# Performance work log

Measured on AMD Instinct MI355X. Metric: run time of the kernel, lower is better.

## Reference

```python
import jax, jax.numpy as jnp
import numpy as np

B, T = 2, 1024
V, D, H, L = 32000, 1024, 16, 8
DH = D // H  # 64
ROPE_BASE = 1000.0
EPS = 1e-6


def _rms_norm(x):
    # F.rms_norm(x, (C,), eps=1e-6)
    ms = jnp.mean(jnp.square(x), axis=-1, keepdims=True)
    return x * jax.lax.rsqrt(ms + EPS)


def _rope_tables(t_len):
    quarter = DH // 4
    inv_freq = jnp.concatenate([
        ROPE_BASE ** (-jnp.arange(quarter, dtype=jnp.float32) / quarter),
        jnp.zeros(quarter, dtype=jnp.float32),
    ])  # [DH/2]
    theta = jnp.arange(t_len, dtype=jnp.float32)[:, None] * inv_freq[None, :]  # [T, DH/2]
    return jnp.cos(theta), jnp.sin(theta)


def _apply_rope(x, cos, sin):
    # x: [B, H, T, DH]; cos/sin: [T, DH/2] broadcast to [1,1,T,DH/2]
    half = DH // 2
    x1, x2 = x[..., :half], x[..., half:]
    c = cos[None, None]
    s = sin[None, None]
    return jnp.concatenate([c * x1 - s * x2, s * x1 + c * x2], axis=-1).astype(x.dtype)


def setup_inputs() -> dict:
    key = jax.random.key(0)
    ks = jax.random.split(key, 7)
    s = 0.02
    return {
        "x_indices": jax.random.randint(ks[0], (B, T), 0, V, dtype=jnp.int32),
        "embedding": jax.random.normal(ks[1], (V, D), dtype=jnp.float32) * s,
        "Wqkv": jax.random.normal(ks[2], (L, 3 * D, D), dtype=jnp.float32) * s,
        "Wout": jax.random.normal(ks[3], (L, D, D), dtype=jnp.float32) * s,
        "W1": jax.random.normal(ks[4], (L, 4 * D, D), dtype=jnp.float32) * s,
        "W2": jax.random.normal(ks[5], (L, D, 4 * D), dtype=jnp.float32) * s,
        "lm_head": jax.random.normal(ks[6], (V, D), dtype=jnp.float32) * s,
    }


def reference(x_indices, embedding, Wqkv, Wout, W1, W2, lm_head):
    x = embedding[x_indices]  # [B, T, D]
    cos, sin = _rope_tables(T)
    causal = jnp.tril(jnp.ones((T, T), dtype=bool))  # [T, T]
    neg = jnp.finfo(x.dtype).min
    scale = 1.0 / np.sqrt(DH)

    for l in range(L):
        n = _rms_norm(x)
        qkv = jnp.einsum('btd,ed->bte', n, Wqkv[l])  # [B, T, 3D]
        qkv = qkv.reshape(B, T, 3, H, DH)
        q = jnp.transpose(qkv[:, :, 0], (0, 2, 1, 3))  # [B, H, T, DH]
        k = jnp.transpose(qkv[:, :, 1], (0, 2, 1, 3))
        v = jnp.transpose(qkv[:, :, 2], (0, 2, 1, 3))
        q = _apply_rope(q, cos, sin)
        k = _apply_rope(k, cos, sin)
        scores = jnp.einsum('bhqd,bhkd->bhqk', q, k) * scale
        scores = jnp.where(causal[None, None], scores, neg)
        attn = jax.nn.softmax(scores, axis=-1)
        ctx = jnp.einsum('bhqk,bhkd->bhqd', attn, v)
        ctx = jnp.transpose(ctx, (0, 2, 1, 3)).reshape(B, T, D)
        x = x + jnp.einsum('btd,ed->bte', ctx, Wout[l])
        n = _rms_norm(x)
        h = jnp.square(jax.nn.relu(jnp.einsum('btd,fd->btf', n, W1[l])))  # [B, T, 4D]
        x = x + jnp.einsum('btf,df->btd', h, W2[l])

    logits = jnp.einsum('btd,vd->btv', _rms_norm(x), lm_head)
    return logits.astype(jnp.float32)
```

## Files before the change

kernel.cpp:

```cpp
#include <hip/hip_runtime.h>
#include <hip/hip_bf16.h>
#include <cmath>
#include <cstdint>

#define B_  2
#define T_  1024
#define V_  32000
#define D_  1024
#define H_  16
#define L_  8
#define DH_ 64

typedef __attribute__((ext_vector_type(8))) short bf16x8;
typedef __attribute__((ext_vector_type(4))) float f32x4;

__device__ __forceinline__ ushort f2bf(float f) {
    union { float f; uint32_t u; } v; v.f = f;
    uint32_t r = v.u + 0x7FFFu + ((v.u >> 16) & 1u);
    return (ushort)(r >> 16);
}
__device__ __forceinline__ float bf2f(ushort u) {
    union { uint32_t u; float f; } v; v.u = ((uint32_t)u) << 16;
    return v.f;
}

__device__ __forceinline__ void async_copy16(const void* g, void* l) {
    __builtin_amdgcn_global_load_lds(
        (const __attribute__((address_space(1))) void*)g,
        (__attribute__((address_space(3))) void*)l, 16, 0, 0);
}

__global__ __launch_bounds__(256) void k_cast(const float4* __restrict__ in,
                                              ushort4* __restrict__ out, int n4) {
    for (int i = blockIdx.x * 256 + threadIdx.x; i < n4; i += gridDim.x * 256) {
        float4 v = in[i];
        out[i] = make_ushort4(f2bf(v.x), f2bf(v.y), f2bf(v.z), f2bf(v.w));
    }
}

__global__ void k_rope_tables(float* __restrict__ cosT, float* __restrict__ sinT) {
    int t = blockIdx.x;
    int i = threadIdx.x;
    float invf = (i < 16) ? powf(1000.0f, -(float)i / 16.0f) : 0.0f;
    float th = (float)t * invf;
    cosT[t * 32 + i] = cosf(th);
    sinT[t * 32 + i] = sinf(th);
}

__global__ __launch_bounds__(256) void k_gather(const int* __restrict__ idx,
                                                const float* __restrict__ emb,
                                                float* __restrict__ x) {
    int row = blockIdx.x;
    int id = idx[row];
    const float4* src = (const float4*)(emb + (size_t)id * D_);
    float4* dst = (float4*)(x + (size_t)row * D_);
    dst[threadIdx.x] = src[threadIdx.x];
}

__global__ __launch_bounds__(256) void k_rmsnorm(const float* __restrict__ x,
                                                 ushort* __restrict__ out) {
    int row = blockIdx.x;
    const float4* xr = (const float4*)(x + (size_t)row * D_);
    float4 v = xr[threadIdx.x];
    float ss = v.x * v.x + v.y * v.y + v.z * v.z + v.w * v.w;
    #pragma unroll
    for (int off = 1; off < 64; off <<= 1) ss += __shfl_xor(ss, off);
    __shared__ float wsum[4];
    int lane = threadIdx.x & 63, wv = threadIdx.x >> 6;
    if (lane == 0) wsum[wv] = ss;
    __syncthreads();
    float tot = wsum[0] + wsum[1] + wsum[2] + wsum[3];
    float inv = rsqrtf(tot * (1.0f / D_) + 1e-6f);
    ushort4 r = make_ushort4(f2bf(v.x * inv), f2bf(v.y * inv), f2bf(v.z * inv), f2bf(v.w * inv));
    *(ushort4*)(out + (size_t)row * D_ + threadIdx.x * 4) = r;
}

template<int BN, int EPI, bool OUTBF, bool CONVB>
__global__ __launch_bounds__(256, 2) void k_mfma_gemm(const ushort* __restrict__ A,
                                                      const void* __restrict__ Wp,
                                                      void* __restrict__ Cp,
                                                      const float* __restrict__ Res,
                                                      const float* __restrict__ cosT,
                                                      const float* __restrict__ sinT,
                                                      int M, int N, int K) {
    constexpr int BM = 128;
    constexpr int MI = 4;
    constexpr int NI = BN / 32;
    constexpr bool DBUF = (BN <= 128);
    constexpr int NB = DBUF ? 2 : 1;
    __shared__ ushort As[NB][BM][64];
    __shared__ ushort Bs[NB][BN][64];
    const int tid = threadIdx.x;
    const int wid = tid >> 6, lane = tid & 63;
    const int wr = wid >> 1, wc = wid & 1;
    const int r16 = lane & 15, kc = lane >> 4;
    const int rx = (r16 & 7) << 4;
    const int srow8 = tid >> 3;
    const int sdcp = tid & 7;

    const int nwg = gridDim.x * gridDim.y;
    int orig = blockIdx.y * gridDim.x + blockIdx.x;
    int swz = (nwg & 7) ? orig : ((orig & 7) * (nwg >> 3) + (orig >> 3));
    const size_t bm = (size_t)(swz % gridDim.x) * BM;
    const size_t bn = (size_t)(swz / gridDim.x) * BN;

    auto stage = [&](int buf, int k0) {
        #pragma unroll
        for (int i = 0; i < 4; i++) {
            const int row = i * 32 + srow8;
            const ushort* g = A + (bm + row) * (size_t)K + k0 + ((sdcp ^ (row & 7)) * 8);
            async_copy16(g, (char*)As + buf * (BM * 128) + (i * 256 + tid) * 16);
        }
        if constexpr (!CONVB) {
            const ushort* Wb = (const ushort*)Wp;
            #pragma unroll
            for (int i = 0; i < BN / 32; i++) {
                const int row = i * 32 + srow8;
                const ushort* g = Wb + (bn + row) * (size_t)K + k0 + ((sdcp ^ (row & 7)) * 8);
                async_copy16(g, (char*)Bs + buf * (BN * 128) + (i * 256 + tid) * 16);
            }
        } else {
            const float* Wf = (const float*)Wp;
            #pragma unroll
            for (int i = 0; i < BN / 32; i++) {
                const int row = i * 32 + srow8;
                const float* src = Wf + (bn + row) * (size_t)K + k0 + sdcp * 8;
                float4 v0 = *(const float4*)(src);
                float4 v1 = *(const float4*)(src + 4);
                union { ushort u[8]; bf16x8 v; } tmp;
                tmp.u[0] = f2bf(v0.x); tmp.u[1] = f2bf(v0.y);
                tmp.u[2] = f2bf(v0.z); tmp.u[3] = f2bf(v0.w);
                tmp.u[4] = f2bf(v1.x); tmp.u[5] = f2bf(v1.y);
                tmp.u[6] = f2bf(v1.z); tmp.u[7] = f2bf(v1.w);
                *(bf16x8*)((char*)Bs + buf * (BN * 128) + row * 128 + ((sdcp ^ (row & 7)) << 4)) = tmp.v;
            }
        }
    };

    f32x4 acc[MI][NI];
    #pragma unroll
    for (int mi = 0; mi < MI; mi++)
        #pragma unroll
        for (int ni = 0; ni < NI; ni++) {
            f32x4 z = {0.f, 0.f, 0.f, 0.f};
            acc[mi][ni] = z;
        }

    auto compute = [&](int buf) {
        #pragma unroll
        for (int kk = 0; kk < 2; kk++) {
            bf16x8 af[MI], bfr[NI];
            #pragma unroll
            for (int mi = 0; mi < MI; mi++)
                af[mi] = *(const bf16x8*)((const char*)As + buf * (BM * 128) +
                                          (wr * 64 + mi * 16 + r16) * 128 +
                                          ((kk * 64 + kc * 16) ^ rx));
            #pragma unroll
            for (int ni = 0; ni < NI; ni++)
                bfr[ni] = *(const bf16x8*)((const char*)Bs + buf * (BN * 128) +
                                           (wc * (BN / 2) + ni * 16 + r16) * 128 +
                                           ((kk * 64 + kc * 16) ^ rx));
            #pragma unroll
            for (int mi = 0; mi < MI; mi++)
                #pragma unroll
                for (int ni = 0; ni < NI; ni++)
                    acc[mi][ni] = __builtin_amdgcn_mfma_f32_16x16x32_bf16(af[mi], bfr[ni],
                                                                          acc[mi][ni], 0, 0, 0);
        }
    };

    const int KSTEPS = K >> 6;
    if constexpr (DBUF) {
        stage(0, 0);
        __syncthreads();
        for (int step = 0; step < KSTEPS; ++step) {
            const int cur = step & 1;
            if (step + 1 < KSTEPS) stage(cur ^ 1, (step + 1) << 6);
            compute(cur);
            __syncthreads();
        }
    } else {
        for (int step = 0; step < KSTEPS; ++step) {
            stage(0, step << 6);
            __syncthreads();
            compute(0);
            __syncthreads();
        }
    }

    #pragma unroll
    for (int mi = 0; mi < MI; mi++) {
        #pragma unroll
        for (int j = 0; j < 4; j++) {
            const size_t row = bm + wr * 64 + mi * 16 + (lane >> 4) * 4 + j;
            if constexpr (EPI == 3) {
                static_assert(BN == 128, "rope epilogue assumes BN=128");
                const int sec = (int)((bn + wc * 64) >> 10);
                if (sec < 2) {
                    const int t = (int)(row & (T_ - 1));
                    #pragma unroll
                    for (int np = 0; np < 2; np++) {
                        const int i1 = np * 16 + r16;
                        float c = cosT[t * 32 + i1], s = sinT[t * 32 + i1];
                        float x1 = acc[mi][np][j], x2 = acc[mi][np + 2][j];
                        acc[mi][np][j]     = c * x1 - s * x2;
                        acc[mi][np + 2][j] = s * x1 + c * x2;
                    }
                }
            }
            #pragma unroll
            for (int ni = 0; ni < NI; ni++) {
                const size_t col = bn + wc * (BN / 2) + ni * 16 + r16;
                float v = acc[mi][ni][j];
                if constexpr (EPI == 1) v += Res[row * N + col];
                if constexpr (EPI == 2) { v = fmaxf(v, 0.f); v *= v; }
                if constexpr (OUTBF) {
                    ((ushort*)Cp)[row * N + col] = f2bf(v);
                } else if constexpr (EPI == 0) {
                    __builtin_nontemporal_store(v, (float*)Cp + row * N + col);
                } else {
                    ((float*)Cp)[row * N + col] = v;
                }
            }
        }
    }
}

__global__ __launch_bounds__(256) void k_attn_mfma(const ushort* __restrict__ qkv,
                                                   ushort* __restrict__ ctx) {
    __shared__ __align__(16) char lds[49152];
    const int tid = threadIdx.x;
    const int w = tid >> 6, lane = tid & 63;
    const int r16 = lane & 15, kc = lane >> 4;
    const int rx = (r16 & 7) << 4;
    const int qb = blockIdx.x * 64;
    const int bh = blockIdx.y, b = bh >> 4, h = bh & 15;
    const size_t tok0 = (size_t)b * T_;
    const ushort* qg = qkv + (tok0 + qb) * (3 * D_) + h * DH_;
    const ushort* kg = qkv + tok0 * (3 * D_) + D_ + h * DH_;
    const ushort* vg = qkv + tok0 * (3 * D_) + 2 * D_ + h * DH_;
    const float SCALE_LOG2E = 0.125f * 1.44269504089f;

    #pragma unroll
    for (int i = 0; i < 2; i++) {
        int slot = i * 256 + tid;
        int row = slot >> 3, dcp = slot & 7;
        int d0 = (dcp ^ (row & 7)) * 8;
        async_copy16(qg + (size_t)row * (3 * D_) + d0, lds + 32768 + slot * 16);
    }
    __syncthreads();
    bf16x8 aq[2];
    #pragma unroll
    for (int ks = 0; ks < 2; ks++) {
        int row = w * 16 + r16;
        aq[ks] = *(const bf16x8*)(lds + 32768 + row * 128 + ((ks * 64 + kc * 16) ^ rx));
    }

    f32x4 o[4];
    float m[4], l[4], corr[4];
    #pragma unroll
    for (int nd = 0; nd < 4; nd++) { f32x4 z = {0.f, 0.f, 0.f, 0.f}; o[nd] = z; }
    #pragma unroll
    for (int j = 0; j < 4; j++) { m[j] = -1e30f; l[j] = 0.f; }

    const int nch = (qb >> 7) + 1;
    for (int ch = 0; ch < nch; ch++) {
        const int kb = ch << 7;
        __syncthreads();
        #pragma unroll
        for (int i = 0; i < 4; i++) {
            int slot = i * 256 + tid;
            int row = slot >> 3, dcp = slot & 7;
            int d0 = (dcp ^ (row & 7)) * 8;
            async_copy16(kg + (size_t)(kb + row) * (3 * D_) + d0, lds + slot * 16);
        }
        #pragma unroll
        for (int r = 0; r < 2; r++) {
            int key = r * 64 + (tid >> 2), dbase = (tid & 3) * 16;
            const ushort* src = vg + (size_t)(kb + key) * (3 * D_) + dbase;
            bf16x8 v0 = *(const bf16x8*)(src);
            bf16x8 v1 = *(const bf16x8*)(src + 8);
            #pragma unroll
            for (int e = 0; e < 8; e++) {
                int d = dbase + e;
                *(ushort*)(lds + 16384 + d * 256 + ((key * 2) ^ ((d & 7) << 4))) = (ushort)v0[e];
                d = dbase + 8 + e;
                *(ushort*)(lds + 16384 + d * 256 + ((key * 2) ^ ((d & 7) << 4))) = (ushort)v1[e];
            }
        }
        __syncthreads();

        f32x4 s[8];
        #pragma unroll
        for (int ni = 0; ni < 8; ni++) { f32x4 z = {0.f, 0.f, 0.f, 0.f}; s[ni] = z; }
        __builtin_amdgcn_s_setprio(1);
        #pragma unroll
        for (int ks = 0; ks < 2; ks++)
            #pragma unroll
            for (int ni = 0; ni < 8; ni++) {
                int row = ni * 16 + r16;
                bf16x8 kf = *(const bf16x8*)(lds + row * 128 + ((ks * 64 + kc * 16) ^ rx));
                s[ni] = __builtin_amdgcn_mfma_f32_16x16x32_bf16(aq[ks], kf, s[ni], 0, 0, 0);
            }
        __builtin_amdgcn_s_setprio(0);

        const bool diag = (ch == nch - 1);
        #pragma unroll
        for (int j = 0; j < 4; j++) {
            const int qrow = qb + w * 16 + kc * 4 + j;
            #pragma unroll
            for (int ni = 0; ni < 8; ni++) {
                float v = s[ni][j] * SCALE_LOG2E;
                if (diag) { int key = kb + ni * 16 + r16; if (key > qrow) v = -1e30f; }
                s[ni][j] = v;
            }
            float t0 = fmaxf(fmaxf(s[0][j], s[1][j]), fmaxf(s[2][j], s[3][j]));
            float t1 = fmaxf(fmaxf(s[4][j], s[5][j]), fmaxf(s[6][j], s[7][j]));
            float t = fmaxf(t0, t1);
            #pragma unroll
            for (int off = 1; off < 16; off <<= 1) t = fmaxf(t, __shfl_xor(t, off));
            float mn = fmaxf(m[j], t);
            corr[j] = exp2f(m[j] - mn);
            m[j] = mn;
            float ps = 0.f;
            #pragma unroll
            for (int ni = 0; ni < 8; ni++) {
                float p = exp2f(s[ni][j] - mn);
                s[ni][j] = p;
                ps += p;
            }
            #pragma unroll
            for (int off = 1; off < 16; off <<= 1) ps += __shfl_xor(ps, off);
            l[j] = l[j] * corr[j] + ps;
        }
        #pragma unroll
        for (int ni = 0; ni < 8; ni++)
            #pragma unroll
            for (int j = 0; j < 4; j++) {
                int row = w * 16 + kc * 4 + j;
                *(ushort*)(lds + 32768 + row * 256 + ((ni * 32 + r16 * 2) ^ ((row & 7) << 4))) = f2bf(s[ni][j]);
            }
        #pragma unroll
        for (int nd = 0; nd < 4; nd++)
            #pragma unroll
            for (int j = 0; j < 4; j++) o[nd][j] *= corr[j];
        __builtin_amdgcn_s_setprio(1);
        #pragma unroll
        for (int ks = 0; ks < 4; ks++) {
            int prow = w * 16 + r16;
            bf16x8 pf = *(const bf16x8*)(lds + 32768 + prow * 256 + ((ks * 64 + kc * 16) ^ rx));
            #pragma unroll
            for (int nd = 0; nd < 4; nd++) {
                int drow = nd * 16 + r16;
                bf16x8 vf = *(const bf16x8*)(lds + 16384 + drow * 256 + ((ks * 64 + kc * 16) ^ rx));
                o[nd] = __builtin_amdgcn_mfma_f32_16x16x32_bf16(pf, vf, o[nd], 0, 0, 0);
            }
        }
        __builtin_amdgcn_s_setprio(0);
    }

    #pragma unroll
    for (int j = 0; j < 4; j++) {
        float inv = 1.0f / l[j];
        int row = qb + w * 16 + kc * 4 + j;
        ushort* dst = ctx + (tok0 + row) * D_ + h * DH_;
        #pragma unroll
        for (int nd = 0; nd < 4; nd++)
            dst[nd * 16 + r16] = f2bf(o[nd][j] * inv);
    }
}

extern "C" void kernel_launch(void* const* d_in, const int* in_sizes, int n_in,
                              void* d_out, int out_size, void* d_ws, size_t ws_size,
                              hipStream_t stream) {
    const int*   xi   = (const int*)d_in[0];
    const float* emb  = (const float*)d_in[1];
    const float* Wqkv = (const float*)d_in[2];
    const float* Wout = (const float*)d_in[3];
    const float* W1   = (const float*)d_in[4];
    const float* W2   = (const float*)d_in[5];
    const float* lmh  = (const float*)d_in[6];
    float* out = (float*)d_out;

    const size_t NT = (size_t)B_ * T_;
    size_t off = 0;
    auto carve = [&](size_t bytes) -> char* {
        char* r = (char*)d_ws + off;
        off += (bytes + 255) & ~(size_t)255;
        return r;
    };
    float*  xbuf = (float*)carve(NT * D_ * 4);
    ushort* qkv  = (ushort*)carve(NT * 3 * D_ * 2);
    ushort* nb   = (ushort*)carve(NT * D_ * 2);
    ushort* ctxb = (ushort*)carve(NT * D_ * 2);
    ushort* hb   = (ushort*)carve(NT * 4 * D_ * 2);
    float*  cosT = (float*)carve(T_ * 32 * 4);
    float*  sinT = (float*)carve(T_ * 32 * 4);

    const size_t nWqkv = (size_t)L_ * 3 * D_ * D_;
    const size_t nWout = (size_t)L_ * D_ * D_;
    const size_t nW1   = (size_t)L_ * 4 * D_ * D_;
    const size_t nW2   = (size_t)L_ * 4 * D_ * D_;
    const size_t nLmh  = (size_t)V_ * D_;
    ushort* WqkvB = (ushort*)carve(nWqkv * 2);
    ushort* WoutB = (ushort*)carve(nWout * 2);
    ushort* W1B   = (ushort*)carve(nW1 * 2);
    ushort* W2B   = (ushort*)carve(nW2 * 2);
    ushort* lmhB  = (ushort*)carve(nLmh * 2);
    const bool preconv = (off <= ws_size);

    if (preconv) {
        k_cast<<<dim3(2048), dim3(256), 0, stream>>>((const float4*)Wqkv, (ushort4*)WqkvB, (int)(nWqkv / 4));
        k_cast<<<dim3(2048), dim3(256), 0, stream>>>((const float4*)Wout, (ushort4*)WoutB, (int)(nWout / 4));
        k_cast<<<dim3(2048), dim3(256), 0, stream>>>((const float4*)W1,   (ushort4*)W1B,   (int)(nW1 / 4));
        k_cast<<<dim3(2048), dim3(256), 0, stream>>>((const float4*)W2,   (ushort4*)W2B,   (int)(nW2 / 4));
        k_cast<<<dim3(2048), dim3(256), 0, stream>>>((const float4*)lmh,  (ushort4*)lmhB,  (int)(nLmh / 4));
    }

#define LAUNCH_GEMM(BN, EPI, OUTBF, GX, GY, Aq, Wb16, Wf32, Cq, Rq, Mv, Nv, Kv)              \
    do {                                                                                     \
        if (preconv)                                                                         \
            k_mfma_gemm<BN, EPI, OUTBF, false><<<dim3(GX, GY), dim3(256), 0, stream>>>(      \
                (const ushort*)(Aq), (const void*)(Wb16), (void*)(Cq), (Rq), cosT, sinT,     \
                Mv, Nv, Kv);                                                                 \
        else                                                                                 \
            k_mfma_gemm<BN, EPI, OUTBF, true><<<dim3(GX, GY), dim3(256), 0, stream>>>(       \
                (const ushort*)(Aq), (const void*)(Wf32), (void*)(Cq), (Rq), cosT, sinT,     \
                Mv, Nv, Kv);                                                                 \
    } while (0)

    k_rope_tables<<<dim3(T_), dim3(32), 0, stream>>>(cosT, sinT);
    k_gather<<<dim3(NT), dim3(256), 0, stream>>>(xi, emb, xbuf);

    for (int l = 0; l < L_; l++) {
        k_rmsnorm<<<dim3(NT), dim3(256), 0, stream>>>(xbuf, nb);
        LAUNCH_GEMM(128, 3, true, 16, 24, nb,
                    WqkvB + (size_t)l * 3 * D_ * D_, Wqkv + (size_t)l * 3 * D_ * D_,
                    qkv, nullptr, (int)NT, 3 * D_, D_);
        k_attn_mfma<<<dim3(T_ / 64, B_ * H_), dim3(256), 0, stream>>>(qkv, ctxb);
        LAUNCH_GEMM(64, 1, false, 16, 16, ctxb,
                    WoutB + (size_t)l * D_ * D_, Wout + (size_t)l * D_ * D_,
                    xbuf, xbuf, (int)NT, D_, D_);
        k_rmsnorm<<<dim3(NT), dim3(256), 0, stream>>>(xbuf, nb);
        LAUNCH_GEMM(128, 2, true, 16, 32, nb,
                    W1B + (size_t)l * 4 * D_ * D_, W1 + (size_t)l * 4 * D_ * D_,
                    hb, nullptr, (int)NT, 4 * D_, D_);
        LAUNCH_GEMM(64, 1, false, 16, 16, hb,
                    W2B + (size_t)l * 4 * D_ * D_, W2 + (size_t)l * 4 * D_ * D_,
                    xbuf, xbuf, (int)NT, D_, 4 * D_);
    }
    k_rmsnorm<<<dim3(NT), dim3(256), 0, stream>>>(xbuf, nb);
    LAUNCH_GEMM(256, 0, false, 16, 125, nb, lmhB, lmh, out, nullptr, (int)NT, V_, D_);
#undef LAUNCH_GEMM
}
```

Before: 1.884 ms.

## Prefetch two K-tiles ahead with counted vmcnt waits in MFMA GEMM

Replaces the one-ahead double-buffered loop with a pipeline that issues global loads two K-steps ahead into a two-slot LDS ring. It uses explicit s_waitcnt vmcnt counts and raw s_barrier, so the loads for the following stage can stay in flight during compute. The single-buffered BN=256 path is removed, and the LM-head GEMM now uses BN=128 with twice as many column blocks so it can use the new pipeline. This depends on the compiler issuing the staged loads in the expected order for the vmcnt counts to be correct, and the smaller LM-head tile reduces reuse.

New measurement: 1.893 ms. About the same (+0.5%).

```diff
diff --git a/kernel.cpp b/kernel.cpp
--- a/kernel.cpp
+++ b/kernel.cpp
@@ -86,10 +86,10 @@
     constexpr int BM = 128;
     constexpr int MI = 4;
     constexpr int NI = BN / 32;
-    constexpr bool DBUF = (BN <= 128);
-    constexpr int NB = DBUF ? 2 : 1;
-    __shared__ ushort As[NB][BM][64];
-    __shared__ ushort Bs[NB][BN][64];
+    constexpr int LOADS = 4 + BN / 32;
+    static_assert(BN <= 128, "dbuf pipeline sized for BN<=128");
+    __shared__ ushort As[2][BM][64];
+    __shared__ ushort Bs[2][BN][64];
     const int tid = threadIdx.x;
     const int wid = tid >> 6, lane = tid & 63;
     const int wr = wid >> 1, wc = wid & 1;
@@ -170,22 +170,32 @@
     };
 
     const int KSTEPS = K >> 6;
-    if constexpr (DBUF) {
-        stage(0, 0);
-        __syncthreads();
-        for (int step = 0; step < KSTEPS; ++step) {
-            const int cur = step & 1;
-            if (step + 1 < KSTEPS) stage(cur ^ 1, (step + 1) << 6);
-            compute(cur);
-            __syncthreads();
-        }
-    } else {
-        for (int step = 0; step < KSTEPS; ++step) {
-            stage(0, step << 6);
-            __syncthreads();
-            compute(0);
-            __syncthreads();
-        }
+    stage(0, 0);
+    stage(1, 64);
+    if constexpr (CONVB)
+        asm volatile("s_waitcnt vmcnt(0) lgkmcnt(0)" ::: "memory");
+    else
+        asm volatile("s_waitcnt vmcnt(%0)" :: "i"(LOADS) : "memory");
+    __builtin_amdgcn_sched_barrier(0);
+    __builtin_amdgcn_s_barrier();
+
+    for (int t = 0; t < KSTEPS; ++t) {
+        compute(t & 1);
+        __builtin_amdgcn_s_barrier();
+        if (t + 2 < KSTEPS) {
+            stage(t & 1, (t + 2) << 6);
+            if constexpr (CONVB)
+                asm volatile("s_waitcnt vmcnt(0) lgkmcnt(0)" ::: "memory");
+            else
+                asm volatile("s_waitcnt vmcnt(%0)" :: "i"(LOADS) : "memory");
+        } else {
+            if constexpr (CONVB)
+                asm volatile("s_waitcnt vmcnt(0) lgkmcnt(0)" ::: "memory");
+            else
+                asm volatile("s_waitcnt vmcnt(0)" ::: "memory");
+        }
+        __builtin_amdgcn_sched_barrier(0);
+        __builtin_amdgcn_s_barrier();
     }
 
     #pragma unroll
@@ -450,6 +460,6 @@
                     xbuf, xbuf, (int)NT, D_, 4 * D_);
     }
     k_rmsnorm<<<dim3(NT), dim3(256), 0, stream>>>(xbuf, nb);
-    LAUNCH_GEMM(256, 0, false, 16, 125, nb, lmhB, lmh, out, nullptr, (int)NT, V_, D_);
+    LAUNCH_GEMM(128, 0, false, 16, 250, nb, lmhB, lmh, out, nullptr, (int)NT, V_, D_);
 #undef LAUNCH_GEMM
 }
```

## Pair causal attention query tiles to balance work and share K/V loads

Applied to the files above, without the earlier changes.

Each attention block now handles two 64-row query tiles, ip and 15-ip, so every block does the same total amount of causal work, and the grid shrinks from 16 to 8 blocks along the query axis. Key/value chunks drop from 128 to 64 keys and are loaded once, then used by both tiles while the chunk is still needed by the lower tile. LDS use falls to 32KB. In exchange there are fewer blocks (256 in total), more per-thread state, and a runtime loop over the active tiles that may hurt unrolling and scheduling.

New measurement: 1.877 ms. About the same (-0.4%).

```diff
diff --git a/kernel.cpp b/kernel.cpp
--- a/kernel.cpp
+++ b/kernel.cpp
@@ -226,148 +226,164 @@
     }
 }
 
-__global__ __launch_bounds__(256) void k_attn_mfma(const ushort* __restrict__ qkv,
+__global__ __launch_bounds__(256) void k_attn_pair(const ushort* __restrict__ qkv,
                                                    ushort* __restrict__ ctx) {
-    __shared__ __align__(16) char lds[49152];
+    __shared__ __align__(16) char lds[32768];
     const int tid = threadIdx.x;
     const int w = tid >> 6, lane = tid & 63;
     const int r16 = lane & 15, kc = lane >> 4;
     const int rx = (r16 & 7) << 4;
-    const int qb = blockIdx.x * 64;
+    const int ip = blockIdx.x;
+    const int qb[2] = { ip * 64, (15 - ip) * 64 };
     const int bh = blockIdx.y, b = bh >> 4, h = bh & 15;
     const size_t tok0 = (size_t)b * T_;
-    const ushort* qg = qkv + (tok0 + qb) * (3 * D_) + h * DH_;
     const ushort* kg = qkv + tok0 * (3 * D_) + D_ + h * DH_;
     const ushort* vg = qkv + tok0 * (3 * D_) + 2 * D_ + h * DH_;
     const float SCALE_LOG2E = 0.125f * 1.44269504089f;
 
     #pragma unroll
-    for (int i = 0; i < 2; i++) {
-        int slot = i * 256 + tid;
-        int row = slot >> 3, dcp = slot & 7;
-        int d0 = (dcp ^ (row & 7)) * 8;
-        async_copy16(qg + (size_t)row * (3 * D_) + d0, lds + 32768 + slot * 16);
+    for (int t = 0; t < 2; t++) {
+        const ushort* qg = qkv + (tok0 + qb[t]) * (3 * D_) + h * DH_;
+        #pragma unroll
+        for (int i = 0; i < 2; i++) {
+            int slot = i * 256 + tid;
+            int row = slot >> 3, dcp = slot & 7;
+            int d0 = (dcp ^ (row & 7)) * 8;
+            async_copy16(qg + (size_t)row * (3 * D_) + d0, lds + 16384 + t * 8192 + slot * 16);
+        }
     }
     __syncthreads();
-    bf16x8 aq[2];
-    #pragma unroll
-    for (int ks = 0; ks < 2; ks++) {
-        int row = w * 16 + r16;
-        aq[ks] = *(const bf16x8*)(lds + 32768 + row * 128 + ((ks * 64 + kc * 16) ^ rx));
-    }
-
-    f32x4 o[4];
-    float m[4], l[4], corr[4];
-    #pragma unroll
-    for (int nd = 0; nd < 4; nd++) { f32x4 z = {0.f, 0.f, 0.f, 0.f}; o[nd] = z; }
-    #pragma unroll
-    for (int j = 0; j < 4; j++) { m[j] = -1e30f; l[j] = 0.f; }
-
-    const int nch = (qb >> 7) + 1;
+    bf16x8 aq[2][2];
+    #pragma unroll
+    for (int t = 0; t < 2; t++)
+        #pragma unroll
+        for (int ks = 0; ks < 2; ks++) {
+            int row = w * 16 + r16;
+            aq[t][ks] = *(const bf16x8*)(lds + 16384 + t * 8192 + row * 128 +
+                                         ((ks * 64 + kc * 16) ^ rx));
+        }
+
+    f32x4 o[2][4];
+    float m[2][4], l[2][4];
+    #pragma unroll
+    for (int t = 0; t < 2; t++)
+        #pragma unroll
+        for (int nd = 0; nd < 4; nd++) {
+            f32x4 z = {0.f, 0.f, 0.f, 0.f};
+            o[t][nd] = z;
+            m[t][nd] = -1e30f; l[t][nd] = 0.f;
+        }
+
+    const int nch = 16 - ip;
     for (int ch = 0; ch < nch; ch++) {
-        const int kb = ch << 7;
+        const int kb = ch << 6;
         __syncthreads();
         #pragma unroll
-        for (int i = 0; i < 4; i++) {
+        for (int i = 0; i < 2; i++) {
             int slot = i * 256 + tid;
             int row = slot >> 3, dcp = slot & 7;
             int d0 = (dcp ^ (row & 7)) * 8;
             async_copy16(kg + (size_t)(kb + row) * (3 * D_) + d0, lds + slot * 16);
         }
-        #pragma unroll
-        for (int r = 0; r < 2; r++) {
-            int key = r * 64 + (tid >> 2), dbase = (tid & 3) * 16;
+        {
+            int key = tid >> 2, dbase = (tid & 3) * 16;
             const ushort* src = vg + (size_t)(kb + key) * (3 * D_) + dbase;
             bf16x8 v0 = *(const bf16x8*)(src);
             bf16x8 v1 = *(const bf16x8*)(src + 8);
             #pragma unroll
             for (int e = 0; e < 8; e++) {
                 int d = dbase + e;
-                *(ushort*)(lds + 16384 + d * 256 + ((key * 2) ^ ((d & 7) << 4))) = (ushort)v0[e];
+                *(ushort*)(lds + 8192 + d * 128 + ((key * 2) ^ ((d & 7) << 4))) = (ushort)v0[e];
                 d = dbase + 8 + e;
-                *(ushort*)(lds + 16384 + d * 256 + ((key * 2) ^ ((d & 7) << 4))) = (ushort)v1[e];
+                *(ushort*)(lds + 8192 + d * 128 + ((key * 2) ^ ((d & 7) << 4))) = (ushort)v1[e];
             }
         }
         __syncthreads();
 
-        f32x4 s[8];
-        #pragma unroll
-        for (int ni = 0; ni < 8; ni++) { f32x4 z = {0.f, 0.f, 0.f, 0.f}; s[ni] = z; }
-        __builtin_amdgcn_s_setprio(1);
-        #pragma unroll
-        for (int ks = 0; ks < 2; ks++)
-            #pragma unroll
-            for (int ni = 0; ni < 8; ni++) {
-                int row = ni * 16 + r16;
-                bf16x8 kf = *(const bf16x8*)(lds + row * 128 + ((ks * 64 + kc * 16) ^ rx));
-                s[ni] = __builtin_amdgcn_mfma_f32_16x16x32_bf16(aq[ks], kf, s[ni], 0, 0, 0);
-            }
-        __builtin_amdgcn_s_setprio(0);
-
-        const bool diag = (ch == nch - 1);
+        const int nact = (ch <= ip) ? 2 : 1;
+        for (int tt = 0; tt < nact; tt++) {
+            const int t = (tt == 0) ? 1 : 0;
+            const int pq = 16384 + t * 8192;
+            f32x4 s[4];
+            #pragma unroll
+            for (int ni = 0; ni < 4; ni++) { f32x4 z = {0.f, 0.f, 0.f, 0.f}; s[ni] = z; }
+            __builtin_amdgcn_s_setprio(1);
+            #pragma unroll
+            for (int ks = 0; ks < 2; ks++)
+                #pragma unroll
+                for (int ni = 0; ni < 4; ni++) {
+                    int row = ni * 16 + r16;
+                    bf16x8 kf = *(const bf16x8*)(lds + row * 128 + ((ks * 64 + kc * 16) ^ rx));
+                    s[ni] = __builtin_amdgcn_mfma_f32_16x16x32_bf16(aq[t][ks], kf, s[ni], 0, 0, 0);
+                }
+            __builtin_amdgcn_s_setprio(0);
+
+            const bool diag = (kb == qb[t]);
+            float corr[4];
+            #pragma unroll
+            for (int j = 0; j < 4; j++) {
+                const int qrow = qb[t] + w * 16 + kc * 4 + j;
+                #pragma unroll
+                for (int ni = 0; ni < 4; ni++) {
+                    float v = s[ni][j] * SCALE_LOG2E;
+                    if (diag) { int key = kb + ni * 16 + r16; if (key > qrow) v = -1e30f; }
+                    s[ni][j] = v;
+                }
+                float tmax = fmaxf(fmaxf(s[0][j], s[1][j]), fmaxf(s[2][j], s[3][j]));
+                #pragma unroll
+                for (int off = 1; off < 16; off <<= 1) tmax = fmaxf(tmax, __shfl_xor(tmax, off));
+                float mn = fmaxf(m[t][j], tmax);
+                corr[j] = exp2f(m[t][j] - mn);
+                m[t][j] = mn;
+                float ps = 0.f;
+                #pragma unroll
+                for (int ni = 0; ni < 4; ni++) {
+                    float p = exp2f(s[ni][j] - mn);
+                    s[ni][j] = p;
+                    ps += p;
+                }
+                #pragma unroll
+                for (int off = 1; off < 16; off <<= 1) ps += __shfl_xor(ps, off);
+                l[t][j] = l[t][j] * corr[j] + ps;
+            }
+            #pragma unroll
+            for (int ni = 0; ni < 4; ni++)
+                #pragma unroll
+                for (int j = 0; j < 4; j++) {
+                    int row = w * 16 + kc * 4 + j;
+                    *(ushort*)(lds + pq + row * 128 + ((ni * 32 + r16 * 2) ^ ((row & 7) << 4))) = f2bf(s[ni][j]);
+                }
+            #pragma unroll
+            for (int nd = 0; nd < 4; nd++)
+                #pragma unroll
+                for (int j = 0; j < 4; j++) o[t][nd][j] *= corr[j];
+            __builtin_amdgcn_s_setprio(1);
+            #pragma unroll
+            for (int ks = 0; ks < 2; ks++) {
+                int prow = w * 16 + r16;
+                bf16x8 pf = *(const bf16x8*)(lds + pq + prow * 128 + ((ks * 64 + kc * 16) ^ rx));
+                #pragma unroll
+                for (int nd = 0; nd < 4; nd++) {
+                    int drow = nd * 16 + r16;
+                    bf16x8 vf = *(const bf16x8*)(lds + 8192 + drow * 128 + ((ks * 64 + kc * 16) ^ rx));
+                    o[t][nd] = __builtin_amdgcn_mfma_f32_16x16x32_bf16(pf, vf, o[t][nd], 0, 0, 0);
+                }
+            }
+            __builtin_amdgcn_s_setprio(0);
+        }
+    }
+
+    #pragma unroll
+    for (int t = 0; t < 2; t++)
         #pragma unroll
         for (int j = 0; j < 4; j++) {
-            const int qrow = qb + w * 16 + kc * 4 + j;
-            #pragma unroll
-            for (int ni = 0; ni < 8; ni++) {
-                float v = s[ni][j] * SCALE_LOG2E;
-                if (diag) { int key = kb + ni * 16 + r16; if (key > qrow) v = -1e30f; }
-                s[ni][j] = v;
-            }
-            float t0 = fmaxf(fmaxf(s[0][j], s[1][j]), fmaxf(s[2][j], s[3][j]));
-            float t1 = fmaxf(fmaxf(s[4][j], s[5][j]), fmaxf(s[6][j], s[7][j]));
-            float t = fmaxf(t0, t1);
-            #pragma unroll
-            for (int off = 1; off < 16; off <<= 1) t = fmaxf(t, __shfl_xor(t, off));
-            float mn = fmaxf(m[j], t);
-            corr[j] = exp2f(m[j] - mn);
-            m[j] = mn;
-            float ps = 0.f;
-            #pragma unroll
-            for (int ni = 0; ni < 8; ni++) {
-                float p = exp2f(s[ni][j] - mn);
-                s[ni][j] = p;
-                ps += p;
-            }
-            #pragma unroll
-            for (int off = 1; off < 16; off <<= 1) ps += __shfl_xor(ps, off);
-            l[j] = l[j] * corr[j] + ps;
-        }
-        #pragma unroll
-        for (int ni = 0; ni < 8; ni++)
-            #pragma unroll
-            for (int j = 0; j < 4; j++) {
-                int row = w * 16 + kc * 4 + j;
-                *(ushort*)(lds + 32768 + row * 256 + ((ni * 32 + r16 * 2) ^ ((row & 7) << 4))) = f2bf(s[ni][j]);
-            }
-        #pragma unroll
-        for (int nd = 0; nd < 4; nd++)
-            #pragma unroll
-            for (int j = 0; j < 4; j++) o[nd][j] *= corr[j];
-        __builtin_amdgcn_s_setprio(1);
-        #pragma unroll
-        for (int ks = 0; ks < 4; ks++) {
-            int prow = w * 16 + r16;
-            bf16x8 pf = *(const bf16x8*)(lds + 32768 + prow * 256 + ((ks * 64 + kc * 16) ^ rx));
-            #pragma unroll
-            for (int nd = 0; nd < 4; nd++) {
-                int drow = nd * 16 + r16;
-                bf16x8 vf = *(const bf16x8*)(lds + 16384 + drow * 256 + ((ks * 64 + kc * 16) ^ rx));
-                o[nd] = __builtin_amdgcn_mfma_f32_16x16x32_bf16(pf, vf, o[nd], 0, 0, 0);
-            }
-        }
-        __builtin_amdgcn_s_setprio(0);
-    }
-
-    #pragma unroll
-    for (int j = 0; j < 4; j++) {
-        float inv = 1.0f / l[j];
-        int row = qb + w * 16 + kc * 4 + j;
-        ushort* dst = ctx + (tok0 + row) * D_ + h * DH_;
-        #pragma unroll
-        for (int nd = 0; nd < 4; nd++)
-            dst[nd * 16 + r16] = f2bf(o[nd][j] * inv);
-    }
+            float inv = 1.0f / l[t][j];
+            int row = qb[t] + w * 16 + kc * 4 + j;
+            ushort* dst = ctx + (tok0 + row) * D_ + h * DH_;
+            #pragma unroll
+            for (int nd = 0; nd < 4; nd++)
+                dst[nd * 16 + r16] = f2bf(o[t][nd][j] * inv);
+        }
 }
 
 extern "C" void kernel_launch(void* const* d_in, const int* in_sizes, int n_in,
@@ -437,7 +453,7 @@
         LAUNCH_GEMM(128, 3, true, 16, 24, nb,
                     WqkvB + (size_t)l * 3 * D_ * D_, Wqkv + (size_t)l * 3 * D_ * D_,
                     qkv, nullptr, (int)NT, 3 * D_, D_);
-        k_attn_mfma<<<dim3(T_ / 64, B_ * H_), dim3(256), 0, stream>>>(qkv, ctxb);
+        k_attn_pair<<<dim3(8, B_ * H_), dim3(256), 0, stream>>>(qkv, ctxb);
         LAUNCH_GEMM(64, 1, false, 16, 16, ctxb,
                     WoutB + (size_t)l * D_ * D_, Wout + (size_t)l * D_ * D_,
                     xbuf, xbuf, (int)NT, D_, D_);
```

## Pair high and low causal query tiles per attention block to balance work

Applied to the files above, without the earlier changes.

Each block now has 512 threads and handles two 64-row query tiles, one from the start and one from the end of the sequence, so every block does roughly the same causal work. The two tiles share each K/V chunk load in LDS, which halves the redundant K/V traffic for the lower tile. Warps on the low tile skip chunks past their causal limit but still take part in loads and barriers. The grid drops to 8x32 blocks with 64KB LDS each, which cuts the number of blocks and may lower occupancy.

New measurement: 1.840 ms. 1.02x faster.

```diff
diff --git a/kernel.cpp b/kernel.cpp
--- a/kernel.cpp
+++ b/kernel.cpp
@@ -226,34 +226,41 @@
     }
 }
 
-__global__ __launch_bounds__(256) void k_attn_mfma(const ushort* __restrict__ qkv,
-                                                   ushort* __restrict__ ctx) {
-    __shared__ __align__(16) char lds[49152];
+__global__ __launch_bounds__(512) void k_attn_p8(const ushort* __restrict__ qkv,
+                                                 ushort* __restrict__ ctx) {
+    __shared__ __align__(16) char lds[65536];
     const int tid = threadIdx.x;
     const int w = tid >> 6, lane = tid & 63;
     const int r16 = lane & 15, kc = lane >> 4;
     const int rx = (r16 & 7) << 4;
-    const int qb = blockIdx.x * 64;
+    const int ip = blockIdx.x;
+    const int tw = w >> 2;
+    const int wq = w & 3;
+    const int hib = (15 - ip) * 64, lob = ip * 64;
+    const int tb = tw ? lob : hib;
+    const int pq = 32768 + tw * 16384;
     const int bh = blockIdx.y, b = bh >> 4, h = bh & 15;
     const size_t tok0 = (size_t)b * T_;
-    const ushort* qg = qkv + (tok0 + qb) * (3 * D_) + h * DH_;
     const ushort* kg = qkv + tok0 * (3 * D_) + D_ + h * DH_;
     const ushort* vg = qkv + tok0 * (3 * D_) + 2 * D_ + h * DH_;
     const float SCALE_LOG2E = 0.125f * 1.44269504089f;
 
-    #pragma unroll
-    for (int i = 0; i < 2; i++) {
-        int slot = i * 256 + tid;
-        int row = slot >> 3, dcp = slot & 7;
-        int d0 = (dcp ^ (row & 7)) * 8;
-        async_copy16(qg + (size_t)row * (3 * D_) + d0, lds + 32768 + slot * 16);
+    {
+        const int bases[2] = { hib, lob };
+        #pragma unroll
+        for (int t = 0; t < 2; t++) {
+            const int row = tid >> 3, dcp = tid & 7;
+            const int d0 = (dcp ^ (row & 7)) * 8;
+            const ushort* qg = qkv + (tok0 + bases[t] + row) * (3 * D_) + h * DH_ + d0;
+            async_copy16(qg, lds + 32768 + t * 16384 + tid * 16);
+        }
     }
     __syncthreads();
     bf16x8 aq[2];
     #pragma unroll
     for (int ks = 0; ks < 2; ks++) {
-        int row = w * 16 + r16;
-        aq[ks] = *(const bf16x8*)(lds + 32768 + row * 128 + ((ks * 64 + kc * 16) ^ rx));
+        const int row = wq * 16 + r16;
+        aq[ks] = *(const bf16x8*)(lds + pq + row * 128 + ((ks * 64 + kc * 16) ^ rx));
     }
 
     f32x4 o[4];
@@ -263,20 +270,19 @@
     #pragma unroll
     for (int j = 0; j < 4; j++) { m[j] = -1e30f; l[j] = 0.f; }
 
-    const int nch = (qb >> 7) + 1;
-    for (int ch = 0; ch < nch; ch++) {
+    const int nchunks = (17 - ip) >> 1;
+    for (int ch = 0; ch < nchunks; ch++) {
         const int kb = ch << 7;
         __syncthreads();
         #pragma unroll
-        for (int i = 0; i < 4; i++) {
-            int slot = i * 256 + tid;
-            int row = slot >> 3, dcp = slot & 7;
-            int d0 = (dcp ^ (row & 7)) * 8;
+        for (int i = 0; i < 2; i++) {
+            const int slot = i * 512 + tid;
+            const int row = slot >> 3, dcp = slot & 7;
+            const int d0 = (dcp ^ (row & 7)) * 8;
             async_copy16(kg + (size_t)(kb + row) * (3 * D_) + d0, lds + slot * 16);
         }
-        #pragma unroll
-        for (int r = 0; r < 2; r++) {
-            int key = r * 64 + (tid >> 2), dbase = (tid & 3) * 16;
+        {
+            const int key = tid >> 2, dbase = (tid & 3) * 16;
             const ushort* src = vg + (size_t)(kb + key) * (3 * D_) + dbase;
             bf16x8 v0 = *(const bf16x8*)(src);
             bf16x8 v1 = *(const bf16x8*)(src + 8);
@@ -290,79 +296,82 @@
         }
         __syncthreads();
 
-        f32x4 s[8];
-        #pragma unroll
-        for (int ni = 0; ni < 8; ni++) { f32x4 z = {0.f, 0.f, 0.f, 0.f}; s[ni] = z; }
-        __builtin_amdgcn_s_setprio(1);
-        #pragma unroll
-        for (int ks = 0; ks < 2; ks++)
-            #pragma unroll
-            for (int ni = 0; ni < 8; ni++) {
-                int row = ni * 16 + r16;
-                bf16x8 kf = *(const bf16x8*)(lds + row * 128 + ((ks * 64 + kc * 16) ^ rx));
-                s[ni] = __builtin_amdgcn_mfma_f32_16x16x32_bf16(aq[ks], kf, s[ni], 0, 0, 0);
-            }
-        __builtin_amdgcn_s_setprio(0);
-
-        const bool diag = (ch == nch - 1);
-        #pragma unroll
-        for (int j = 0; j < 4; j++) {
-            const int qrow = qb + w * 16 + kc * 4 + j;
-            #pragma unroll
-            for (int ni = 0; ni < 8; ni++) {
-                float v = s[ni][j] * SCALE_LOG2E;
-                if (diag) { int key = kb + ni * 16 + r16; if (key > qrow) v = -1e30f; }
-                s[ni][j] = v;
-            }
-            float t0 = fmaxf(fmaxf(s[0][j], s[1][j]), fmaxf(s[2][j], s[3][j]));
-            float t1 = fmaxf(fmaxf(s[4][j], s[5][j]), fmaxf(s[6][j], s[7][j]));
-            float t = fmaxf(t0, t1);
-            #pragma unroll
-            for (int off = 1; off < 16; off <<= 1) t = fmaxf(t, __shfl_xor(t, off));
-            float mn = fmaxf(m[j], t);
-            corr[j] = exp2f(m[j] - mn);
-            m[j] = mn;
-            float ps = 0.f;
-            #pragma unroll
-            for (int ni = 0; ni < 8; ni++) {
-                float p = exp2f(s[ni][j] - mn);
-                s[ni][j] = p;
-                ps += p;
-            }
-            #pragma unroll
-            for (int off = 1; off < 16; off <<= 1) ps += __shfl_xor(ps, off);
-            l[j] = l[j] * corr[j] + ps;
-        }
-        #pragma unroll
-        for (int ni = 0; ni < 8; ni++)
+        const bool active = (tw == 0) || (kb < lob + 64);
+        if (active) {
+            f32x4 s[8];
+            #pragma unroll
+            for (int ni = 0; ni < 8; ni++) { f32x4 z = {0.f, 0.f, 0.f, 0.f}; s[ni] = z; }
+            __builtin_amdgcn_s_setprio(1);
+            #pragma unroll
+            for (int ks = 0; ks < 2; ks++)
+                #pragma unroll
+                for (int ni = 0; ni < 8; ni++) {
+                    const int row = ni * 16 + r16;
+                    bf16x8 kf = *(const bf16x8*)(lds + row * 128 + ((ks * 64 + kc * 16) ^ rx));
+                    s[ni] = __builtin_amdgcn_mfma_f32_16x16x32_bf16(aq[ks], kf, s[ni], 0, 0, 0);
+                }
+            __builtin_amdgcn_s_setprio(0);
+
+            const bool needmask = (kb + 127 > tb);
             #pragma unroll
             for (int j = 0; j < 4; j++) {
-                int row = w * 16 + kc * 4 + j;
-                *(ushort*)(lds + 32768 + row * 256 + ((ni * 32 + r16 * 2) ^ ((row & 7) << 4))) = f2bf(s[ni][j]);
-            }
-        #pragma unroll
-        for (int nd = 0; nd < 4; nd++)
-            #pragma unroll
-            for (int j = 0; j < 4; j++) o[nd][j] *= corr[j];
-        __builtin_amdgcn_s_setprio(1);
-        #pragma unroll
-        for (int ks = 0; ks < 4; ks++) {
-            int prow = w * 16 + r16;
-            bf16x8 pf = *(const bf16x8*)(lds + 32768 + prow * 256 + ((ks * 64 + kc * 16) ^ rx));
-            #pragma unroll
-            for (int nd = 0; nd < 4; nd++) {
-                int drow = nd * 16 + r16;
-                bf16x8 vf = *(const bf16x8*)(lds + 16384 + drow * 256 + ((ks * 64 + kc * 16) ^ rx));
-                o[nd] = __builtin_amdgcn_mfma_f32_16x16x32_bf16(pf, vf, o[nd], 0, 0, 0);
-            }
-        }
-        __builtin_amdgcn_s_setprio(0);
+                const int qrow = tb + wq * 16 + kc * 4 + j;
+                #pragma unroll
+                for (int ni = 0; ni < 8; ni++) {
+                    float v = s[ni][j] * SCALE_LOG2E;
+                    if (needmask) { int key = kb + ni * 16 + r16; if (key > qrow) v = -1e30f; }
+                    s[ni][j] = v;
+                }
+                float t0 = fmaxf(fmaxf(s[0][j], s[1][j]), fmaxf(s[2][j], s[3][j]));
+                float t1 = fmaxf(fmaxf(s[4][j], s[5][j]), fmaxf(s[6][j], s[7][j]));
+                float tmax = fmaxf(t0, t1);
+                #pragma unroll
+                for (int off = 1; off < 16; off <<= 1) tmax = fmaxf(tmax, __shfl_xor(tmax, off));
+                const float mn = fmaxf(m[j], tmax);
+                corr[j] = exp2f(m[j] - mn);
+                m[j] = mn;
+                float ps = 0.f;
+                #pragma unroll
+                for (int ni = 0; ni < 8; ni++) {
+                    float p = exp2f(s[ni][j] - mn);
+                    s[ni][j] = p;
+                    ps += p;
+                }
+                #pragma unroll
+                for (int off = 1; off < 16; off <<= 1) ps += __shfl_xor(ps, off);
+                l[j] = l[j] * corr[j] + ps;
+            }
+            #pragma unroll
+            for (int ni = 0; ni < 8; ni++)
+                #pragma unroll
+                for (int j = 0; j < 4; j++) {
+                    const int row = wq * 16 + kc * 4 + j;
+                    *(ushort*)(lds + pq + row * 256 + ((ni * 32 + r16 * 2) ^ ((row & 7) << 4))) = f2bf(s[ni][j]);
+                }
+            #pragma unroll
+            for (int nd = 0; nd < 4; nd++)
+                #pragma unroll
+                for (int j = 0; j < 4; j++) o[nd][j] *= corr[j];
+            __builtin_amdgcn_s_setprio(1);
+            #pragma unroll
+            for (int ks = 0; ks < 4; ks++) {
+                const int prow = wq * 16 + r16;
+                bf16x8 pf = *(const bf16x8*)(lds + pq + prow * 256 + ((ks * 64 + kc * 16) ^ rx));
+                #pragma unroll
+                for (int nd = 0; nd < 4; nd++) {
+                    const int drow = nd * 16 + r16;
+                    bf16x8 vf = *(const bf16x8*)(lds + 16384 + drow * 256 + ((ks * 64 + kc * 16) ^ rx));
+                    o[nd] = __builtin_amdgcn_mfma_f32_16x16x32_bf16(pf, vf, o[nd], 0, 0, 0);
+                }
+            }
+            __builtin_amdgcn_s_setprio(0);
+        }
     }
 
     #pragma unroll
     for (int j = 0; j < 4; j++) {
-        float inv = 1.0f / l[j];
-        int row = qb + w * 16 + kc * 4 + j;
+        const float inv = 1.0f / l[j];
+        const int row = tb + wq * 16 + kc * 4 + j;
         ushort* dst = ctx + (tok0 + row) * D_ + h * DH_;
         #pragma unroll
         for (int nd = 0; nd < 4; nd++)
@@ -437,7 +446,7 @@
         LAUNCH_GEMM(128, 3, true, 16, 24, nb,
                     WqkvB + (size_t)l * 3 * D_ * D_, Wqkv + (size_t)l * 3 * D_ * D_,
                     qkv, nullptr, (int)NT, 3 * D_, D_);
-        k_attn_mfma<<<dim3(T_ / 64, B_ * H_), dim3(256), 0, stream>>>(qkv, ctxb);
+        k_attn_p8<<<dim3(8, B_ * H_), dim3(512), 0, stream>>>(qkv, ctxb);
         LAUNCH_GEMM(64, 1, false, 16, 16, ctxb,
                     WoutB + (size_t)l * D_ * D_, Wout + (size_t)l * D_ * D_,
                     xbuf, xbuf, (int)NT, D_, D_);
```
